# Optimization experiments

Hardware: AMD Instinct MI355X
Metric: run time of the kernel (lower is better)

## Reference

```python
import jax, jax.numpy as jnp
import numpy as np

B, T, U = 4, 250, 120
EPROJS, DUNITS, EMBED, JOINT, ODIM, ATT = 512, 512, 512, 512, 1024, 512
BLANK = 0


def _p(key, shape, scale=0.02):
    return jax.random.normal(key, shape, dtype=jnp.float32) * scale


def setup_inputs() -> dict:
    key = jax.random.key(0)
    ks = jax.random.split(key, 24)
    hs_pad = jax.random.normal(ks[0], (B, T, EPROJS), dtype=jnp.float32)
    ys_in_pad = jax.random.randint(ks[1], (B, U), 0, ODIM)
    hlens = jax.random.randint(ks[2], (B,), T // 2, T + 1).astype(jnp.int32)
    embed = _p(ks[3], (ODIM, EMBED)).at[BLANK].set(0.0)  # padding_idx=blank
    # LSTMCell layer 0: input = embed + eprojs
    W_ih0 = _p(ks[4], (4 * DUNITS, EMBED + EPROJS)); b_ih0 = jnp.zeros((4 * DUNITS,), jnp.float32)
    W_hh0 = _p(ks[5], (4 * DUNITS, DUNITS));          b_hh0 = jnp.zeros((4 * DUNITS,), jnp.float32)
    # LSTMCell layer 1
    W_ih1 = _p(ks[6], (4 * DUNITS, DUNITS)); b_ih1 = jnp.zeros((4 * DUNITS,), jnp.float32)
    W_hh1 = _p(ks[7], (4 * DUNITS, DUNITS)); b_hh1 = jnp.zeros((4 * DUNITS,), jnp.float32)
    # additive attention (AttAdd): mlp_enc (bias), mlp_dec (no bias), gvec
    W_att_enc = _p(ks[8], (EPROJS, ATT)); b_att_enc = jnp.zeros((ATT,), jnp.float32)
    W_att_dec = _p(ks[9], (DUNITS, ATT))
    gvec = _p(ks[10], (ATT,))
    # joint network
    W_lin_enc = _p(ks[11], (JOINT, EPROJS)); b_lin_enc = jnp.zeros((JOINT,), jnp.float32)
    W_lin_dec = _p(ks[12], (JOINT, DUNITS))  # bias=False
    W_lin_out = _p(ks[13], (ODIM, JOINT));   b_lin_out = jnp.zeros((ODIM,), jnp.float32)
    return dict(hs_pad=hs_pad, ys_in_pad=ys_in_pad, hlens=hlens, embed=embed,
                W_ih0=W_ih0, b_ih0=b_ih0, W_hh0=W_hh0, b_hh0=b_hh0,
                W_ih1=W_ih1, b_ih1=b_ih1, W_hh1=W_hh1, b_hh1=b_hh1,
                W_att_enc=W_att_enc, b_att_enc=b_att_enc, W_att_dec=W_att_dec, gvec=gvec,
                W_lin_enc=W_lin_enc, b_lin_enc=b_lin_enc, W_lin_dec=W_lin_dec,
                W_lin_out=W_lin_out, b_lin_out=b_lin_out)


def _lstm_cell(x, h, c, W_ih, b_ih, W_hh, b_hh):
    g = x @ W_ih.T + b_ih + h @ W_hh.T + b_hh
    i, f, gg, o = jnp.split(g, 4, axis=-1)  # torch gate order: i, f, g, o
    c_new = jax.nn.sigmoid(f) * c + jax.nn.sigmoid(i) * jnp.tanh(gg)
    h_new = jax.nn.sigmoid(o) * jnp.tanh(c_new)
    return h_new, c_new


def reference(hs_pad, ys_in_pad, hlens, embed,
              W_ih0, b_ih0, W_hh0, b_hh0, W_ih1, b_ih1, W_hh1, b_hh1,
              W_att_enc, b_att_enc, W_att_dec, gvec,
              W_lin_enc, b_lin_enc, W_lin_dec, W_lin_out, b_lin_out):
    Bq, Tq = hs_pad.shape[0], hs_pad.shape[1]
    eys = embed[ys_in_pad]  # (B, U, E)
    pre_enc = hs_pad @ W_att_enc + b_att_enc  # (B, T, A), computed once
    mask = jnp.arange(Tq)[None, :] < hlens[:, None]  # (B, T)

    def step(carry, ey_i):
        z0, c0, z1, c1 = carry
        # additive attention: scores over encoder frames
        q = z0 @ W_att_dec  # (B, A)
        e = jnp.tanh(pre_enc + q[:, None, :]) @ gvec  # (B, T)
        e = jnp.where(mask, e, -1e9)
        w = jax.nn.softmax(e, axis=-1)
        att_c = jnp.einsum('bt,btd->bd', w, hs_pad)  # (B, eprojs)
        ey = jnp.concatenate([ey_i, att_c], axis=1)  # (B, E+eprojs)
        z0n, c0n = _lstm_cell(ey, z0, c0, W_ih0, b_ih0, W_hh0, b_hh0)
        z1n, c1n = _lstm_cell(z0n, z1, c1, W_ih1, b_ih1, W_hh1, b_hh1)
        return (z0n, c0n, z1n, c1n), z1n

    zeros = jnp.zeros((Bq, DUNITS), hs_pad.dtype)
    _, ys = jax.lax.scan(step, (zeros, zeros, zeros, zeros),
                         jnp.swapaxes(eys, 0, 1))  # ys: (U, B, D)
    h_dec = jnp.swapaxes(ys, 0, 1)  # (B, U, D)

    # joint: broadcast add of enc/dec projections, tanh, output proj
    henc = hs_pad @ W_lin_enc.T + b_lin_enc  # (B, T, J)
    hdec = h_dec @ W_lin_dec.T               # (B, U, J)
    z = jnp.tanh(henc[:, :, None, :] + hdec[:, None, :, :])  # (B, T, U, J)
    return z @ W_lin_out.T + b_lin_out  # (B, T, U, odim)
```

## Files before the change

kernel.cpp:

```cpp
#include <hip/hip_runtime.h>

#define B_ 4
#define T_ 250
#define U_ 120
#define D_ 512
#define G_ 2048
#define O_ 1024
#define NBLK 256

typedef __attribute__((ext_vector_type(8))) short bf16x8;
typedef __attribute__((ext_vector_type(4))) float f32x4;
typedef __attribute__((ext_vector_type(4))) unsigned int ui4;

__device__ __forceinline__ float tanh_fast(float x){
  float e = __expf(2.f*x);
  return 1.f - 2.f/(e + 1.f);
}
__device__ __forceinline__ float sigmoid_fast(float x){
  return 1.f/(1.f + __expf(-x));
}
__device__ __forceinline__ unsigned short f2bf(float x){
  unsigned int u = __float_as_uint(x);
  unsigned int r = (u + 0x7FFFu + ((u >> 16) & 1u)) >> 16;
  return (unsigned short)r;
}

__device__ __forceinline__ void atomStoreF(float* p, float v){
  __hip_atomic_store(p, v, __ATOMIC_RELAXED, __HIP_MEMORY_SCOPE_AGENT);
}
__device__ __forceinline__ void mall_load4f(const float* p0, const float* p1,
    const float* p2, const float* p3, float& v0, float& v1, float& v2, float& v3){
  asm volatile(
    "global_load_dword %0, %4, off sc0 sc1\n\t"
    "global_load_dword %1, %5, off sc0 sc1\n\t"
    "global_load_dword %2, %6, off sc0 sc1\n\t"
    "global_load_dword %3, %7, off sc0 sc1\n\t"
    "s_waitcnt vmcnt(0)"
    : "=&v"(v0), "=&v"(v1), "=&v"(v2), "=&v"(v3)
    : "v"(p0), "v"(p1), "v"(p2), "v"(p3)
    : "memory");
}

__device__ __forceinline__ void gbar_arrive(int* flags, int gen){
  __syncthreads();
  if (threadIdx.x == 0){
    asm volatile("s_waitcnt vmcnt(0)" ::: "memory");
    __hip_atomic_store(&flags[blockIdx.x*16], gen, __ATOMIC_RELAXED,
                       __HIP_MEMORY_SCOPE_AGENT);
  }
}
__device__ __forceinline__ void gbar_wait(int* flags, int* rel, int gen){
  if (blockIdx.x == 0){
    if (threadIdx.x < 64){
      int l = threadIdx.x;
      const int* p0 = flags + (l*4+0)*16;
      const int* p1 = flags + (l*4+1)*16;
      const int* p2 = flags + (l*4+2)*16;
      const int* p3 = flags + (l*4+3)*16;
      long c = 0;
      while (true){
        int f0,f1,f2,f3;
        asm volatile(
          "global_load_dword %0, %4, off sc0 sc1\n\t"
          "global_load_dword %1, %5, off sc0 sc1\n\t"
          "global_load_dword %2, %6, off sc0 sc1\n\t"
          "global_load_dword %3, %7, off sc0 sc1\n\t"
          "s_waitcnt vmcnt(0)"
          : "=&v"(f0),"=&v"(f1),"=&v"(f2),"=&v"(f3)
          : "v"(p0), "v"(p1), "v"(p2), "v"(p3)
          : "memory");
        int m0 = f0 < f1 ? f0 : f1;
        int m1 = f2 < f3 ? f2 : f3;
        int mm = m0 < m1 ? m0 : m1;
        if (__all(mm >= gen)) break;
        if (++c > (1L<<22)) break;
      }
      if (threadIdx.x == 0)
        __hip_atomic_store(rel, gen, __ATOMIC_RELAXED,
                           __HIP_MEMORY_SCOPE_AGENT);
    }
  } else {
    if (threadIdx.x == 0){
      long c = 0;
      while (__hip_atomic_load(rel, __ATOMIC_RELAXED,
                               __HIP_MEMORY_SCOPE_AGENT) < gen){
        if (++c > (1L<<22)) break;
      }
    }
  }
  __syncthreads();
}
__device__ __forceinline__ void gbar(int* flags, int* rel, int gen){
  gbar_arrive(flags, gen);
  gbar_wait(flags, rel, gen);
}

__global__ void barinit_k(int* flags){
  int i = blockIdx.x*256 + threadIdx.x;
  if (i < NBLK*16 + 16)
    __hip_atomic_store(&flags[i], 0, __ATOMIC_RELAXED, __HIP_MEMORY_SCOPE_AGENT);
}

__global__ void gather_embed_k(const int* __restrict__ ys, const float* __restrict__ embed,
                               float* __restrict__ eys){
  int i = blockIdx.x*256 + threadIdx.x;
  if (i < B_*U_*D_){
    int r = i >> 9, k = i & 511;
    eys[i] = embed[ys[r]*D_ + k];
  }
}

__device__ __forceinline__ void gemm64_nt_body(float* smem,
  const float* __restrict__ A, int lda, const float* __restrict__ B, int ldb,
  const float* __restrict__ bias, float* __restrict__ C, int ldc,
  int M, int N, int K, int bx, int by)
{
  float (*As)[65] = (float(*)[65])smem;
  float (*Bs)[65] = (float(*)[65])(smem + 16*65);
  int tid = threadIdx.x;
  int m0 = by*64, n0 = bx*64;
  int tx = tid & 15, ty = tid >> 4;
  float acc[4][4] = {};
  for (int k0 = 0; k0 < K; k0 += 16){
#pragma unroll
    for (int i=0;i<4;i++){
      int e = tid + 256*i;
      int mm = e >> 4, kk = e & 15;
      int mg = m0 + mm;
      As[kk][mm] = (mg < M) ? A[(size_t)mg*lda + k0 + kk] : 0.f;
      int ng = n0 + mm;
      Bs[kk][mm] = (ng < N) ? B[(size_t)ng*ldb + k0 + kk] : 0.f;
    }
    __syncthreads();
#pragma unroll
    for (int kk=0;kk<16;kk++){
      float av[4], bv[4];
#pragma unroll
      for (int i=0;i<4;i++) av[i] = As[kk][ty*4+i];
#pragma unroll
      for (int j=0;j<4;j++) bv[j] = Bs[kk][tx*4+j];
#pragma unroll
      for (int i=0;i<4;i++)
#pragma unroll
        for (int j=0;j<4;j++) acc[i][j] += av[i]*bv[j];
    }
    __syncthreads();
  }
#pragma unroll
  for (int i=0;i<4;i++){
    int m = m0 + ty*4 + i;
    if (m < M){
#pragma unroll
      for (int j=0;j<4;j++){
        int n = n0 + tx*4 + j;
        if (n < N) C[(size_t)m*ldc + n] = acc[i][j] + (bias ? bias[n] : 0.f);
      }
    }
  }
}

__device__ __forceinline__ void gemm64_nn_body(float* smem,
  const float* __restrict__ A, int lda, const float* __restrict__ B, int ldb,
  const float* __restrict__ bias, float* __restrict__ C, int ldc,
  int M, int N, int K, int bx, int by)
{
  float (*As)[65] = (float(*)[65])smem;
  float (*Bs)[65] = (float(*)[65])(smem + 16*65);
  int tid = threadIdx.x;
  int m0 = by*64, n0 = bx*64;
  int tx = tid & 15, ty = tid >> 4;
  float acc[4][4] = {};
  for (int k0 = 0; k0 < K; k0 += 16){
#pragma unroll
    for (int i=0;i<4;i++){
      int e = tid + 256*i;
      int mm = e >> 4, kk = e & 15;
      int mg = m0 + mm;
      As[kk][mm] = (mg < M) ? A[(size_t)mg*lda + k0 + kk] : 0.f;
      int nn = e & 63, kk2 = e >> 6;
      int ng = n0 + nn;
      Bs[kk2][nn] = (ng < N) ? B[(size_t)(k0+kk2)*ldb + ng] : 0.f;
    }
    __syncthreads();
#pragma unroll
    for (int kk=0;kk<16;kk++){
      float av[4], bv[4];
#pragma unroll
      for (int i=0;i<4;i++) av[i] = As[kk][ty*4+i];
#pragma unroll
      for (int j=0;j<4;j++) bv[j] = Bs[kk][tx*4+j];
#pragma unroll
      for (int i=0;i<4;i++)
#pragma unroll
        for (int j=0;j<4;j++) acc[i][j] += av[i]*bv[j];
    }
    __syncthreads();
  }
#pragma unroll
  for (int i=0;i<4;i++){
    int m = m0 + ty*4 + i;
    if (m < M){
#pragma unroll
      for (int j=0;j<4;j++){
        int n = n0 + tx*4 + j;
        if (n < N) C[(size_t)m*ldc + n] = acc[i][j] + (bias ? bias[n] : 0.f);
      }
    }
  }
}

__global__ __launch_bounds__(256) void pre_gemms_k(
  const float* __restrict__ hs, const float* __restrict__ eys,
  const float* __restrict__ W_att_enc, const float* __restrict__ b_att_enc,
  const float* __restrict__ W_lin_enc, const float* __restrict__ b_lin_enc,
  const float* __restrict__ W_ih0,
  float* __restrict__ pre_enc, float* __restrict__ henc,
  float* __restrict__ pre0, float* __restrict__ hsW0)
{
  __shared__ float smem[2*16*65];
  int id = blockIdx.x;
  if (id < 128){
    gemm64_nn_body(smem, hs,512, W_att_enc,512, b_att_enc, pre_enc,512,
                   B_*T_,512,512, id & 7, id >> 3);
  } else if (id < 256){
    id -= 128;
    gemm64_nt_body(smem, hs,512, W_lin_enc,512, b_lin_enc, henc,512,
                   B_*T_,512,512, id & 7, id >> 3);
  } else if (id < 512){
    id -= 256;
    gemm64_nt_body(smem, eys,512, W_ih0,1024, nullptr, pre0,2048,
                   B_*U_,2048,512, id & 31, id >> 5);
  } else {
    id -= 512;
    gemm64_nt_body(smem, hs,512, W_ih0+512,1024, nullptr, hsW0,2048,
                   B_*T_,2048,512, id & 31, id >> 5);
  }
}

__global__ __launch_bounds__(256) void gemm64_nt_k(
  const float* __restrict__ A, int lda, const float* __restrict__ B, int ldb,
  const float* __restrict__ bias, float* __restrict__ C, int ldc,
  int M, int N, int K)
{
  __shared__ float smem[2*16*65];
  gemm64_nt_body(smem, A,lda,B,ldb,bias,C,ldc,M,N,K, blockIdx.x, blockIdx.y);
}

__global__ __launch_bounds__(256) void scan_k(
    float* __restrict__ z0, float* __restrict__ z1,
    float* __restrict__ q,  float* __restrict__ e,
    int* __restrict__ flags, int* __restrict__ rel,
    const float* __restrict__ pre_enc, const float* __restrict__ pre0,
    const float* __restrict__ hsW0,
    const float* __restrict__ W_hh0, const float* __restrict__ W_ih1,
    const float* __restrict__ W_hh1, const float* __restrict__ W_att_dec,
    const float* __restrict__ gvec, const int* __restrict__ hlens,
    const float* __restrict__ b_ih0, const float* __restrict__ b_hh0,
    const float* __restrict__ b_ih1, const float* __restrict__ b_hh1,
    float* __restrict__ h_dec)
{
  int bk = blockIdx.x, tid = threadIdx.x;
  int lane = tid & 63, wv = tid >> 6;
  int d0 = bk * 2;

  __shared__ float whh0_s[8*512];
  __shared__ float whh1_s[8*512];
  __shared__ float wih1_s[8*512];
  __shared__ float wdec_s[2*512];
  __shared__ float hsw_s[4*8*256];
  __shared__ float pre0_s[480*8];
  __shared__ float pre_s[4*512];
  __shared__ float gvec_s[512];
  __shared__ float zs0[2048], zs1[2048], qs[2048];
  __shared__ float pA0[32], pA1[32], gB[32], gC[32];
  __shared__ float bias0_s[8], bias1_s[8], c0_s[8], c1_s[8];
  __shared__ int hlens_s[4];

  for (int idx = tid; idx < 8*512; idx += 256){
    int gd = idx >> 9, k = idx & 511;
    int j = (gd >> 1)*512 + d0 + (gd & 1);
    whh0_s[idx] = W_hh0[(size_t)j*512 + k];
    whh1_s[idx] = W_hh1[(size_t)j*512 + k];
    wih1_s[idx] = W_ih1[(size_t)j*512 + k];
  }
  for (int idx = tid; idx < 2*512; idx += 256){
    int dd = idx >> 9, k = idx & 511;
    wdec_s[idx] = W_att_dec[(size_t)k*512 + d0 + dd];
  }
  for (int idx = tid; idx < 4*1000; idx += 256){
    int gp = idx & 3, tg = idx >> 2;
    int b = tg / 250, t = tg - b*250;
    const float2 v = *(const float2*)(hsW0 + (size_t)tg*G_ + gp*512 + d0);
    hsw_s[(b*8 + gp*2 + 0)*256 + t] = v.x;
    hsw_s[(b*8 + gp*2 + 1)*256 + t] = v.y;
  }
  for (int idx = tid; idx < 4*8*6; idx += 256){
    int t = 250 + (idx % 6), bg = idx / 6;
    hsw_s[bg*256 + t] = 0.f;
  }
  for (int idx = tid; idx < 480*4; idx += 256){
    int gp = idx & 3, r = idx >> 2;
    const float2 v = *(const float2*)(pre0 + (size_t)r*G_ + gp*512 + d0);
    pre0_s[r*8 + gp*2 + 0] = v.x;
    pre0_s[r*8 + gp*2 + 1] = v.y;
  }
  for (int idx = tid; idx < 4*512; idx += 256){
    int r = bk*4 + (idx >> 9);
    pre_s[idx] = (r < B_*T_) ? pre_enc[(size_t)r*512 + (idx & 511)] : 0.f;
  }
  for (int idx = tid; idx < 512; idx += 256) gvec_s[idx] = gvec[idx];
  for (int idx = tid; idx < 2048; idx += 256) zs0[idx] = 0.f;
  if (tid < 4) hlens_s[tid] = hlens[tid];
  if (tid < 32){ pA0[tid] = 0.f; }
  if (tid < 8){
    int j = ((tid >> 1))*512 + d0 + (tid & 1);
    bias0_s[tid] = b_ih0[j] + b_hh0[j];
    bias1_s[tid] = b_ih1[j] + b_hh1[j];
    c0_s[tid] = 0.f; c1_s[tid] = 0.f;
    int b = tid >> 1, d = d0 + (tid & 1);
    atomStoreF(&z1[b*512 + d], 0.f);
    atomStoreF(&q [b*512 + d], 0.f);
  }
  int gen = 0;
  gbar(flags, rel, ++gen);

  for (int u = 0; u < U_; ++u){
    {
      float vz[8], vq[8];
#pragma unroll
      for (int i=0;i<8;i++)
        asm volatile("global_load_dword %0, %1, off sc0 sc1"
                     : "=&v"(vz[i]) : "v"(&z1[tid + 256*i]));
#pragma unroll
      for (int i=0;i<8;i++)
        asm volatile("global_load_dword %0, %1, off sc0 sc1"
                     : "=&v"(vq[i]) : "v"(&q[tid + 256*i]));
      asm volatile("s_waitcnt vmcnt(0)" ::: "memory");
#pragma unroll
      for (int i=0;i<8;i++){ zs1[tid + 256*i] = vz[i]; qs[tid + 256*i] = vq[i]; }
    }
    __syncthreads();
    {
      int r = bk*4 + wv;
      if (r < B_*T_){
        int b = r / 250, t = r - b*250;
        float s = 0.f;
#pragma unroll
        for (int i=0;i<8;i++){
          int k = i*64 + lane;
          float x = pre_s[wv*512+k] + qs[b*512+k];
          s += tanh_fast(x) * gvec_s[k];
        }
#pragma unroll
        for (int off=32; off; off>>=1) s += __shfl_xor(s, off);
        if (lane == 0) atomStoreF(&e[r], (t < hlens_s[b]) ? s : -1e30f);
      }
    }
    gbar_arrive(flags, ++gen);
    {
      int gd0 = wv*2, gd1 = wv*2 + 1;
      float a10[4]={}, a11[4]={};
#pragma unroll
      for (int i = 0; i < 8; ++i){
        int k = i*64 + lane;
        float w10 = whh1_s[gd0*512+k], w11 = whh1_s[gd1*512+k];
#pragma unroll
        for (int b=0;b<4;b++){
          float zv1 = zs1[b*512+k];
          a10[b] += w10*zv1; a11[b] += w11*zv1;
        }
      }
#pragma unroll
      for (int b=0;b<4;b++){
#pragma unroll
        for (int off=32; off; off>>=1){
          a10[b] += __shfl_xor(a10[b],off); a11[b] += __shfl_xor(a11[b],off);
        }
      }
      if (lane == 0){
#pragma unroll
        for (int b=0;b<4;b++){ pA1[b*8+gd0] = a10[b]; pA1[b*8+gd1] = a11[b]; }
      }
    }
    gbar_wait(flags, rel, gen);
    {
      int b = wv;
      const float* eb = e + b*250;
      float vals[4], w_reg[4];
      int t3 = 192 + lane;
      mall_load4f(eb + lane, eb + 64 + lane, eb + 128 + lane,
                  eb + (t3 < 250 ? t3 : 249),
                  vals[0], vals[1], vals[2], vals[3]);
      if (t3 >= 250) vals[3] = -1e30f;
      float vmax = fmaxf(fmaxf(vals[0],vals[1]), fmaxf(vals[2],vals[3]));
#pragma unroll
      for (int off=32; off; off>>=1) vmax = fmaxf(vmax, __shfl_xor(vmax, off));
      float ssum = 0.f;
#pragma unroll
      for (int i=0;i<4;i++){
        int t = i*64 + lane;
        w_reg[i] = (t < 250) ? __expf(vals[i] - vmax) : 0.f;
        ssum += w_reg[i];
      }
#pragma unroll
      for (int off=32; off; off>>=1) ssum += __shfl_xor(ssum, off);
      float inv = 1.f / ssum;
#pragma unroll
      for (int i=0;i<4;i++) w_reg[i] *= inv;

      float ag[8] = {};
#pragma unroll
      for (int i=0;i<4;i++){
        int t = i*64 + lane;
#pragma unroll
        for (int gd=0; gd<8; gd++)
          ag[gd] += w_reg[i] * hsw_s[(b*8+gd)*256 + t];
      }
#pragma unroll
      for (int gd=0; gd<8; gd++){
#pragma unroll
        for (int off=32; off; off>>=1) ag[gd] += __shfl_xor(ag[gd], off);
      }
      if (lane == 0){
#pragma unroll
        for (int gd=0; gd<8; gd++)
          gB[b*8+gd] = ag[gd] + pA0[b*8+gd] + pre0_s[(b*U_+u)*8 + gd] + bias0_s[gd];
      }
    }
    __syncthreads();
    if (tid < 8){
      int b = tid >> 1, dd = tid & 1;
      float ig = sigmoid_fast(gB[b*8 + 0 + dd]);
      float fg = sigmoid_fast(gB[b*8 + 2 + dd]);
      float gg = tanh_fast  (gB[b*8 + 4 + dd]);
      float og = sigmoid_fast(gB[b*8 + 6 + dd]);
      float cn = fg * c0_s[tid] + ig * gg;
      c0_s[tid] = cn;
      atomStoreF(&z0[b*512 + d0 + dd], og * tanh_fast(cn));
    }
    gbar(flags, rel, ++gen);
    {
      float vza[8];
#pragma unroll
      for (int i=0;i<8;i++)
        asm volatile("global_load_dword %0, %1, off sc0 sc1"
                     : "=&v"(vza[i]) : "v"(&z0[tid + 256*i]));
      asm volatile("s_waitcnt vmcnt(0)" ::: "memory");
#pragma unroll
      for (int i=0;i<8;i++) zs0[tid + 256*i] = vza[i];
    }
    __syncthreads();
    {
      int gd0 = wv*2, gd1 = wv*2 + 1;
      float a0[4]={}, a1[4]={};
#pragma unroll
      for (int i=0;i<8;i++){
        int k = i*64 + lane;
        float w0 = wih1_s[gd0*512+k], w1 = wih1_s[gd1*512+k];
#pragma unroll
        for (int b=0;b<4;b++){
          float zv = zs0[b*512+k];
          a0[b] += w0*zv; a1[b] += w1*zv;
        }
      }
#pragma unroll
      for (int b=0;b<4;b++){
#pragma unroll
        for (int off=32; off; off>>=1){
          a0[b] += __shfl_xor(a0[b],off); a1[b] += __shfl_xor(a1[b],off);
        }
      }
      if (lane == 0){
#pragma unroll
        for (int b=0;b<4;b++){
          gC[b*8+gd0] = a0[b] + pA1[b*8+gd0] + bias1_s[gd0];
          gC[b*8+gd1] = a1[b] + pA1[b*8+gd1] + bias1_s[gd1];
        }
      }
      if (wv < 2){
        float qa[4] = {};
#pragma unroll
        for (int i=0;i<8;i++){
          int k = i*64 + lane;
          float wq = wdec_s[wv*512+k];
#pragma unroll
          for (int b=0;b<4;b++) qa[b] += wq * zs0[b*512+k];
        }
#pragma unroll
        for (int b=0;b<4;b++){
#pragma unroll
          for (int off=32; off; off>>=1) qa[b] += __shfl_xor(qa[b],off);
        }
        if (lane == 0){
#pragma unroll
          for (int b=0;b<4;b++) atomStoreF(&q[b*512 + d0 + wv], qa[b]);
        }
      }
    }
    __syncthreads();
    if (tid < 8){
      int b = tid >> 1, dd = tid & 1;
      float ig = sigmoid_fast(gC[b*8 + 0 + dd]);
      float fg = sigmoid_fast(gC[b*8 + 2 + dd]);
      float gg = tanh_fast  (gC[b*8 + 4 + dd]);
      float og = sigmoid_fast(gC[b*8 + 6 + dd]);
      float cn = fg * c1_s[tid] + ig * gg;
      c1_s[tid] = cn;
      float hn = og * tanh_fast(cn);
      atomStoreF(&z1[b*512 + d0 + dd], hn);
      h_dec[((size_t)(b*U_ + u))*512 + d0 + dd] = hn;
    }
    gbar_arrive(flags, ++gen);
    {
      int gd0 = wv*2, gd1 = wv*2 + 1;
      float a00[4]={}, a01[4]={};
#pragma unroll
      for (int i = 0; i < 8; ++i){
        int k = i*64 + lane;
        float w00 = whh0_s[gd0*512+k], w01 = whh0_s[gd1*512+k];
#pragma unroll
        for (int b=0;b<4;b++){
          float zv0 = zs0[b*512+k];
          a00[b] += w00*zv0; a01[b] += w01*zv0;
        }
      }
#pragma unroll
      for (int b=0;b<4;b++){
#pragma unroll
        for (int off=32; off; off>>=1){
          a00[b] += __shfl_xor(a00[b],off); a01[b] += __shfl_xor(a01[b],off);
        }
      }
      if (lane == 0){
#pragma unroll
        for (int b=0;b<4;b++){ pA0[b*8+gd0] = a00[b]; pA0[b*8+gd1] = a01[b]; }
      }
    }
    gbar_wait(flags, rel, gen);
  }
}

__global__ __launch_bounds__(256) void pack_k(
    const float* __restrict__ henc, const float* __restrict__ hdec,
    unsigned short* __restrict__ P,
    const float* __restrict__ Wlin, unsigned short* __restrict__ Wb)
{
  const int NP8 = B_*T_*U_*512/8;
  int i = blockIdx.x*256 + threadIdx.x;
  if (i < NP8){
    int e = i*8;
    int k = e & 511;
    int r = e >> 9;
    int u = r % U_;
    int bt = r / U_;
    int b = bt / T_;
    const float* hp = henc + (size_t)bt*512 + k;
    const float* dp = hdec + (size_t)(b*U_ + u)*512 + k;
    unsigned int w[4];
#pragma unroll
    for (int j=0;j<4;j++){
      unsigned short lo = f2bf(tanh_fast(hp[2*j]   + dp[2*j]));
      unsigned short hi = f2bf(tanh_fast(hp[2*j+1] + dp[2*j+1]));
      w[j] = (unsigned int)lo | ((unsigned int)hi << 16);
    }
    *(ui4*)(P + e) = ui4{w[0], w[1], w[2], w[3]};
  } else {
    int j8 = i - NP8;
    if (j8 < O_*512/8){
      int e = j8*8;
      unsigned int w[4];
#pragma unroll
      for (int j=0;j<4;j++){
        unsigned short lo = f2bf(Wlin[e+2*j]);
        unsigned short hi = f2bf(Wlin[e+2*j+1]);
        w[j] = (unsigned int)lo | ((unsigned int)hi << 16);
      }
      *(ui4*)(Wb + e) = ui4{w[0], w[1], w[2], w[3]};
    }
  }
}

__global__ __launch_bounds__(256) void joint_mfma_k(
    const unsigned short* __restrict__ P,
    const unsigned short* __restrict__ Wb,
    const float* __restrict__ bout,
    float* __restrict__ out)
{
  __shared__ __align__(16) char smraw[32768];
  unsigned short* As = (unsigned short*)smraw;
  unsigned short* Bs = (unsigned short*)(smraw + 16384);
  float* outb = (float*)smraw;
  int tid = threadIdx.x;
  int lane = tid & 63;
  int w = tid >> 6, wr = w >> 1, wc = w & 1;
  int id = blockIdx.x;
  int bt = id % 1000;
  int ot = id / 1000;
  int o0 = ot * 128;
  const char* Pbase = (const char*)(P + (size_t)bt*U_*512);
  const char* Wbase = (const char*)(Wb + (size_t)o0*512);

  f32x4 acc[4][4] = {};

  for (int k0 = 0; k0 < 512; k0 += 64){
    __syncthreads();
#pragma unroll
    for (int j=0;j<4;j++){
      int pos = (j*256 + tid)*16;
      int row = pos >> 7;
      int inrow = pos & 127;
      int srcin = inrow ^ ((row & 7) << 4);
      int arow = row < U_ ? row : (U_-1);
      __builtin_amdgcn_global_load_lds(
        (const __attribute__((address_space(1))) void*)(Pbase + (size_t)arow*1024 + k0*2 + srcin),
        (__attribute__((address_space(3))) void*)((char*)As + pos), 16, 0, 0);
      __builtin_amdgcn_global_load_lds(
        (const __attribute__((address_space(1))) void*)(Wbase + (size_t)row*1024 + k0*2 + srcin),
        (__attribute__((address_space(3))) void*)((char*)Bs + pos), 16, 0, 0);
    }
    __syncthreads();
#pragma unroll
    for (int kk=0; kk<2; kk++){
      bf16x8 a[4], bb[4];
#pragma unroll
      for (int m=0;m<4;m++){
        int row = wr*64 + m*16 + (lane & 15);
        int inrow = (kk*64 + (lane >> 4)*16) ^ ((row & 7) << 4);
        a[m] = *(const bf16x8*)((const char*)As + row*128 + inrow);
      }
#pragma unroll
      for (int n=0;n<4;n++){
        int row = wc*64 + n*16 + (lane & 15);
        int inrow = (kk*64 + (lane >> 4)*16) ^ ((row & 7) << 4);
        bb[n] = *(const bf16x8*)((const char*)Bs + row*128 + inrow);
      }
#pragma unroll
      for (int m=0;m<4;m++)
#pragma unroll
        for (int n=0;n<4;n++)
          acc[m][n] = __builtin_amdgcn_mfma_f32_16x16x32_bf16(a[m], bb[n], acc[m][n], 0, 0, 0);
    }
  }
  float bv[4];
#pragma unroll
  for (int n=0;n<4;n++) bv[n] = bout[o0 + wc*64 + n*16 + (lane & 15)];
#pragma unroll
  for (int m=0;m<4;m++){
    __syncthreads();
#pragma unroll
    for (int n=0;n<4;n++){
      int col = wc*64 + n*16 + (lane & 15);
      int r0 = wr*16 + ((lane >> 4) << 2);
#pragma unroll
      for (int r=0;r<4;r++)
        outb[(r0+r)*132 + col] = acc[m][n][r] + bv[n];
    }
    __syncthreads();
    int row = tid >> 3;
    int c0  = (tid & 7) * 16;
    int u = (row < 16) ? (m*16 + row) : (64 + m*16 + (row - 16));
    if (u < U_){
      float* op = out + ((size_t)bt*U_ + u)*O_ + o0 + c0;
      const float* sp = &outb[row*132 + c0];
#pragma unroll
      for (int i=0;i<4;i++) *(f32x4*)(op + 4*i) = *(const f32x4*)(sp + 4*i);
    }
  }
}

extern "C" void kernel_launch(void* const* d_in, const int* in_sizes, int n_in,
                              void* d_out, int out_size, void* d_ws, size_t ws_size,
                              hipStream_t stream) {
  const float* hs       = (const float*)d_in[0];
  const int*   ys       = (const int*)  d_in[1];
  const int*   hlens    = (const int*)  d_in[2];
  const float* embed    = (const float*)d_in[3];
  const float* W_ih0    = (const float*)d_in[4];
  const float* b_ih0    = (const float*)d_in[5];
  const float* W_hh0    = (const float*)d_in[6];
  const float* b_hh0    = (const float*)d_in[7];
  const float* W_ih1    = (const float*)d_in[8];
  const float* b_ih1    = (const float*)d_in[9];
  const float* W_hh1    = (const float*)d_in[10];
  const float* b_hh1    = (const float*)d_in[11];
  const float* W_att_enc= (const float*)d_in[12];
  const float* b_att_enc= (const float*)d_in[13];
  const float* W_att_dec= (const float*)d_in[14];
  const float* gvec     = (const float*)d_in[15];
  const float* W_lin_enc= (const float*)d_in[16];
  const float* b_lin_enc= (const float*)d_in[17];
  const float* W_lin_dec= (const float*)d_in[18];
  const float* W_lin_out= (const float*)d_in[19];
  const float* b_lin_out= (const float*)d_in[20];
  float* out = (float*)d_out;

  float* w = (float*)d_ws;
  float* z0      = w;
  float* z1      = w + 2048;
  float* q       = w + 4096;
  float* e       = w + 6144;
  int*   flags   = (int*)(w + 7168);
  int*   rel     = flags + NBLK*16;
  float* eys     = w + 11776;
  float* pre_enc = w + 257536;
  float* pre0    = w + 769536;
  float* henc    = w + 1752576;
  float* h_dec   = w + 2264576;
  float* hdec_p  = w + 2510336;
  float* hsW0    = w + 2756096;
  unsigned short* Pbf = (unsigned short*)(w + 4804096);
  unsigned short* Wbf = (unsigned short*)(w + 4804096 + 30720000);

  barinit_k<<<17, 256, 0, stream>>>(flags);
  gather_embed_k<<<(B_*U_*D_ + 255)/256, 256, 0, stream>>>(ys, embed, eys);
  pre_gemms_k<<<1024, 256, 0, stream>>>(hs, eys, W_att_enc, b_att_enc,
                                        W_lin_enc, b_lin_enc, W_ih0,
                                        pre_enc, henc, pre0, hsW0);

  {
    void* args[] = {
      (void*)&z0, (void*)&z1, (void*)&q, (void*)&e, (void*)&flags, (void*)&rel,
      (void*)&pre_enc, (void*)&pre0, (void*)&hsW0,
      (void*)&W_hh0, (void*)&W_ih1, (void*)&W_hh1, (void*)&W_att_dec,
      (void*)&gvec, (void*)&hlens,
      (void*)&b_ih0, (void*)&b_hh0, (void*)&b_ih1, (void*)&b_hh1,
      (void*)&h_dec
    };
    hipLaunchCooperativeKernel((const void*)scan_k, dim3(NBLK), dim3(256),
                               args, 0, stream);
  }

  gemm64_nt_k<<<dim3(8, 8), 256, 0, stream>>>(h_dec, 512, W_lin_dec, 512, nullptr,
                                              hdec_p, 512, B_*U_, 512, 512);
  {
    const int NP8 = B_*T_*U_*512/8;
    const int NW8 = O_*512/8;
    pack_k<<<(NP8 + NW8 + 255)/256, 256, 0, stream>>>(henc, hdec_p, Pbf,
                                                      W_lin_out, Wbf);
  }
  joint_mfma_k<<<8000, 256, 0, stream>>>(Pbf, Wbf, b_lin_out, out);
}
```

Measured before the change: 1.909 ms.

## Enlarge pre-GEMM tiles, merge barrier init, and trim per-step scan loads

The pre-scan GEMMs move from 64x64 to 128x128 tiles with 8x8 per-thread accumulators, which cuts the launch from 1024 blocks to 256. Barrier-flag initialisation is folded into the embedding gather kernel, removing one launch. In the scan loop, each block now loads only the q rows for the batches it covers, and the z1 loads are left in flight during the attention score computation before being waited on. The larger tiles raise register pressure and lower parallelism in the GEMM phase. The scan changes target per-step latency on the serial critical path.

```diff
diff --git a/kernel.cpp b/kernel.cpp
--- a/kernel.cpp
+++ b/kernel.cpp
@@ -95,15 +95,11 @@
   gbar_wait(flags, rel, gen);
 }
 
-__global__ void barinit_k(int* flags){
+__global__ void gather_embed_k(const int* __restrict__ ys, const float* __restrict__ embed,
+                               float* __restrict__ eys, int* __restrict__ flags){
   int i = blockIdx.x*256 + threadIdx.x;
   if (i < NBLK*16 + 16)
     __hip_atomic_store(&flags[i], 0, __ATOMIC_RELAXED, __HIP_MEMORY_SCOPE_AGENT);
-}
-
-__global__ void gather_embed_k(const int* __restrict__ ys, const float* __restrict__ embed,
-                               float* __restrict__ eys){
-  int i = blockIdx.x*256 + threadIdx.x;
   if (i < B_*U_*D_){
     int r = i >> 9, k = i & 511;
     eys[i] = embed[ys[r]*D_ + k];
@@ -159,50 +155,98 @@
   }
 }
 
-__device__ __forceinline__ void gemm64_nn_body(float* smem,
+__device__ __forceinline__ void gemm128_nt_body(float* smem,
   const float* __restrict__ A, int lda, const float* __restrict__ B, int ldb,
   const float* __restrict__ bias, float* __restrict__ C, int ldc,
   int M, int N, int K, int bx, int by)
 {
-  float (*As)[65] = (float(*)[65])smem;
-  float (*Bs)[65] = (float(*)[65])(smem + 16*65);
+  float (*As)[129] = (float(*)[129])smem;
+  float (*Bs)[129] = (float(*)[129])(smem + 16*129);
   int tid = threadIdx.x;
-  int m0 = by*64, n0 = bx*64;
+  int m0 = by*128, n0 = bx*128;
   int tx = tid & 15, ty = tid >> 4;
-  float acc[4][4] = {};
+  float acc[8][8] = {};
   for (int k0 = 0; k0 < K; k0 += 16){
 #pragma unroll
-    for (int i=0;i<4;i++){
+    for (int i=0;i<8;i++){
+      int e = tid + 256*i;
+      int mm = e >> 4, kk = e & 15;
+      int mg = m0 + mm, ng = n0 + mm;
+      As[kk][mm] = (mg < M) ? A[(size_t)mg*lda + k0 + kk] : 0.f;
+      Bs[kk][mm] = (ng < N) ? B[(size_t)ng*ldb + k0 + kk] : 0.f;
+    }
+    __syncthreads();
+#pragma unroll
+    for (int kk=0;kk<16;kk++){
+      float av[8], bv[8];
+#pragma unroll
+      for (int i=0;i<8;i++) av[i] = As[kk][ty*8+i];
+#pragma unroll
+      for (int j=0;j<8;j++) bv[j] = Bs[kk][tx*8+j];
+#pragma unroll
+      for (int i=0;i<8;i++)
+#pragma unroll
+        for (int j=0;j<8;j++) acc[i][j] += av[i]*bv[j];
+    }
+    __syncthreads();
+  }
+#pragma unroll
+  for (int i=0;i<8;i++){
+    int m = m0 + ty*8 + i;
+    if (m < M){
+#pragma unroll
+      for (int j=0;j<8;j++){
+        int n = n0 + tx*8 + j;
+        if (n < N) C[(size_t)m*ldc + n] = acc[i][j] + (bias ? bias[n] : 0.f);
+      }
+    }
+  }
+}
+
+__device__ __forceinline__ void gemm128_nn_body(float* smem,
+  const float* __restrict__ A, int lda, const float* __restrict__ B, int ldb,
+  const float* __restrict__ bias, float* __restrict__ C, int ldc,
+  int M, int N, int K, int bx, int by)
+{
+  float (*As)[129] = (float(*)[129])smem;
+  float (*Bs)[129] = (float(*)[129])(smem + 16*129);
+  int tid = threadIdx.x;
+  int m0 = by*128, n0 = bx*128;
+  int tx = tid & 15, ty = tid >> 4;
+  float acc[8][8] = {};
+  for (int k0 = 0; k0 < K; k0 += 16){
+#pragma unroll
+    for (int i=0;i<8;i++){
       int e = tid + 256*i;
       int mm = e >> 4, kk = e & 15;
       int mg = m0 + mm;
       As[kk][mm] = (mg < M) ? A[(size_t)mg*lda + k0 + kk] : 0.f;
-      int nn = e & 63, kk2 = e >> 6;
+      int nn = e & 127, kk2 = e >> 7;
       int ng = n0 + nn;
       Bs[kk2][nn] = (ng < N) ? B[(size_t)(k0+kk2)*ldb + ng] : 0.f;
     }
     __syncthreads();
 #pragma unroll
     for (int kk=0;kk<16;kk++){
-      float av[4], bv[4];
-#pragma unroll
-      for (int i=0;i<4;i++) av[i] = As[kk][ty*4+i];
-#pragma unroll
-      for (int j=0;j<4;j++) bv[j] = Bs[kk][tx*4+j];
-#pragma unroll
-      for (int i=0;i<4;i++)
-#pragma unroll
-        for (int j=0;j<4;j++) acc[i][j] += av[i]*bv[j];
-    }
-    __syncthreads();
-  }
-#pragma unroll
-  for (int i=0;i<4;i++){
-    int m = m0 + ty*4 + i;
+      float av[8], bv[8];
+#pragma unroll
+      for (int i=0;i<8;i++) av[i] = As[kk][ty*8+i];
+#pragma unroll
+      for (int j=0;j<8;j++) bv[j] = Bs[kk][tx*8+j];
+#pragma unroll
+      for (int i=0;i<8;i++)
+#pragma unroll
+        for (int j=0;j<8;j++) acc[i][j] += av[i]*bv[j];
+    }
+    __syncthreads();
+  }
+#pragma unroll
+  for (int i=0;i<8;i++){
+    int m = m0 + ty*8 + i;
     if (m < M){
 #pragma unroll
-      for (int j=0;j<4;j++){
-        int n = n0 + tx*4 + j;
+      for (int j=0;j<8;j++){
+        int n = n0 + tx*8 + j;
         if (n < N) C[(size_t)m*ldc + n] = acc[i][j] + (bias ? bias[n] : 0.f);
       }
     }
@@ -217,23 +261,23 @@
   float* __restrict__ pre_enc, float* __restrict__ henc,
   float* __restrict__ pre0, float* __restrict__ hsW0)
 {
-  __shared__ float smem[2*16*65];
+  __shared__ float smem[2*16*129];
   int id = blockIdx.x;
-  if (id < 128){
-    gemm64_nn_body(smem, hs,512, W_att_enc,512, b_att_enc, pre_enc,512,
-                   B_*T_,512,512, id & 7, id >> 3);
-  } else if (id < 256){
+  if (id < 32){
+    gemm128_nn_body(smem, hs,512, W_att_enc,512, b_att_enc, pre_enc,512,
+                    B_*T_,512,512, id & 3, id >> 2);
+  } else if (id < 64){
+    id -= 32;
+    gemm128_nt_body(smem, hs,512, W_lin_enc,512, b_lin_enc, henc,512,
+                    B_*T_,512,512, id & 3, id >> 2);
+  } else if (id < 128){
+    id -= 64;
+    gemm128_nt_body(smem, eys,512, W_ih0,1024, nullptr, pre0,2048,
+                    B_*U_,2048,512, id & 15, id >> 4);
+  } else {
     id -= 128;
-    gemm64_nt_body(smem, hs,512, W_lin_enc,512, b_lin_enc, henc,512,
-                   B_*T_,512,512, id & 7, id >> 3);
-  } else if (id < 512){
-    id -= 256;
-    gemm64_nt_body(smem, eys,512, W_ih0,1024, nullptr, pre0,2048,
-                   B_*U_,2048,512, id & 31, id >> 5);
-  } else {
-    id -= 512;
-    gemm64_nt_body(smem, hs,512, W_ih0+512,1024, nullptr, hsW0,2048,
-                   B_*T_,2048,512, id & 31, id >> 5);
+    gemm128_nt_body(smem, hs,512, W_ih0+512,1024, nullptr, hsW0,2048,
+                    B_*T_,2048,512, id & 15, id >> 4);
   }
 }
 
@@ -276,6 +320,9 @@
   __shared__ float bias0_s[8], bias1_s[8], c0_s[8], c1_s[8];
   __shared__ int hlens_s[4];
 
+  int b_lo = (bk*4) / 250;     if (b_lo > 3) b_lo = 3;
+  int b_hi = (bk*4 + 3) / 250; if (b_hi > 3) b_hi = 3;
+
   for (int idx = tid; idx < 8*512; idx += 256){
     int gd = idx >> 9, k = idx & 511;
     int j = (gd >> 1)*512 + d0 + (gd & 1);
@@ -325,19 +372,36 @@
   gbar(flags, rel, ++gen);
 
   for (int u = 0; u < U_; ++u){
+    float vq0,vq1,vq2,vq3;
+    float vz0,vz1,vz2,vz3,vz4,vz5,vz6,vz7;
     {
-      float vz[8], vq[8];
-#pragma unroll
-      for (int i=0;i<8;i++)
-        asm volatile("global_load_dword %0, %1, off sc0 sc1"
-                     : "=&v"(vz[i]) : "v"(&z1[tid + 256*i]));
-#pragma unroll
-      for (int i=0;i<8;i++)
-        asm volatile("global_load_dword %0, %1, off sc0 sc1"
-                     : "=&v"(vq[i]) : "v"(&q[tid + 256*i]));
-      asm volatile("s_waitcnt vmcnt(0)" ::: "memory");
-#pragma unroll
-      for (int i=0;i<8;i++){ zs1[tid + 256*i] = vz[i]; qs[tid + 256*i] = vq[i]; }
+      const float* qa = &q[b_lo*512 + tid*2];
+      const float* qb = &q[b_hi*512 + tid*2];
+      asm volatile(
+        "global_load_dword %0, %12, off sc0 sc1\n\t"
+        "global_load_dword %1, %13, off sc0 sc1\n\t"
+        "global_load_dword %2, %14, off sc0 sc1\n\t"
+        "global_load_dword %3, %15, off sc0 sc1\n\t"
+        "global_load_dword %4, %16, off sc0 sc1\n\t"
+        "global_load_dword %5, %17, off sc0 sc1\n\t"
+        "global_load_dword %6, %18, off sc0 sc1\n\t"
+        "global_load_dword %7, %19, off sc0 sc1\n\t"
+        "global_load_dword %8, %20, off sc0 sc1\n\t"
+        "global_load_dword %9, %21, off sc0 sc1\n\t"
+        "global_load_dword %10, %22, off sc0 sc1\n\t"
+        "global_load_dword %11, %23, off sc0 sc1\n\t"
+        "s_waitcnt vmcnt(8)"
+        : "=&v"(vq0),"=&v"(vq1),"=&v"(vq2),"=&v"(vq3),
+          "=&v"(vz0),"=&v"(vz1),"=&v"(vz2),"=&v"(vz3),
+          "=&v"(vz4),"=&v"(vz5),"=&v"(vz6),"=&v"(vz7)
+        : "v"(qa), "v"(qa+1), "v"(qb), "v"(qb+1),
+          "v"(&z1[tid]), "v"(&z1[tid+256]), "v"(&z1[tid+512]), "v"(&z1[tid+768]),
+          "v"(&z1[tid+1024]), "v"(&z1[tid+1280]), "v"(&z1[tid+1536]), "v"(&z1[tid+1792])
+        : "memory");
+      qs[b_lo*512 + tid*2]     = vq0;
+      qs[b_lo*512 + tid*2 + 1] = vq1;
+      qs[b_hi*512 + tid*2]     = vq2;
+      qs[b_hi*512 + tid*2 + 1] = vq3;
     }
     __syncthreads();
     {
@@ -356,6 +420,12 @@
         if (lane == 0) atomStoreF(&e[r], (t < hlens_s[b]) ? s : -1e30f);
       }
     }
+    asm volatile("s_waitcnt vmcnt(0)"
+      : "+v"(vz0),"+v"(vz1),"+v"(vz2),"+v"(vz3),
+        "+v"(vz4),"+v"(vz5),"+v"(vz6),"+v"(vz7) :: "memory");
+    __builtin_amdgcn_sched_barrier(0);
+    zs1[tid]      = vz0; zs1[tid+256]  = vz1; zs1[tid+512]  = vz2; zs1[tid+768]  = vz3;
+    zs1[tid+1024] = vz4; zs1[tid+1280] = vz5; zs1[tid+1536] = vz6; zs1[tid+1792] = vz7;
     gbar_arrive(flags, ++gen);
     {
       int gd0 = wv*2, gd1 = wv*2 + 1;
@@ -711,11 +781,10 @@
   unsigned short* Pbf = (unsigned short*)(w + 4804096);
   unsigned short* Wbf = (unsigned short*)(w + 4804096 + 30720000);
 
-  barinit_k<<<17, 256, 0, stream>>>(flags);
-  gather_embed_k<<<(B_*U_*D_ + 255)/256, 256, 0, stream>>>(ys, embed, eys);
-  pre_gemms_k<<<1024, 256, 0, stream>>>(hs, eys, W_att_enc, b_att_enc,
-                                        W_lin_enc, b_lin_enc, W_ih0,
-                                        pre_enc, henc, pre0, hsW0);
+  gather_embed_k<<<(B_*U_*D_ + 255)/256, 256, 0, stream>>>(ys, embed, eys, flags);
+  pre_gemms_k<<<256, 256, 0, stream>>>(hs, eys, W_att_enc, b_att_enc,
+                                       W_lin_enc, b_lin_enc, W_ih0,
+                                       pre_enc, henc, pre0, hsW0);
 
   {
     void* args[] = {
```

Result: slower. 1.979 ms (+3.6%).
